# Kernel optimization log

Hardware: AMD Instinct MI355X
Metric: run time of the kernel (lower is better)

Reference implementation:

```python
import jax, jax.numpy as jnp
import numpy as np

PASS = 8        # pass_through_size
FLOW = 16       # flow_size
TRANS = FLOW - PASS  # transform_size = 8
NBINS = 64
HID = 1024


def _conditioner(yA, w1, b1, w2, b2, w3, b3):
    # MLP producing unnormalized positive bin widths Q: [B, TRANS, NBINS]
    h = jax.nn.relu(yA @ w1 + b1)
    h = jax.nn.relu(h @ w2 + b2)
    q = jax.nn.softplus(h @ w3 + b3) + 1e-6  # positivity for slopes
    return q.reshape(-1, TRANS, NBINS)


def setup_inputs() -> dict:
    key = jax.random.key(0)
    ks = jax.random.split(key, 4)
    B = 65536
    y = jax.random.uniform(ks[0], (B, FLOW + 1), dtype=jnp.float32)
    w1 = jax.random.normal(ks[1], (PASS, HID), dtype=jnp.float32) / np.sqrt(PASS)
    w2 = jax.random.normal(ks[2], (HID, HID), dtype=jnp.float32) / np.sqrt(HID)
    w3 = jax.random.normal(ks[3], (HID, TRANS * NBINS), dtype=jnp.float32) / np.sqrt(HID)
    return {
        "y": y,
        "w1": w1, "b1": jnp.zeros((HID,), jnp.float32),
        "w2": w2, "b2": jnp.zeros((HID,), jnp.float32),
        "w3": w3, "b3": jnp.zeros((TRANS * NBINS,), jnp.float32),
    }


def reference(y, w1, b1, w2, b2, w3, b3):
    yA = y[:, :PASS]                      # [B, PASS]
    yB = y[:, PASS:FLOW]                  # [B, TRANS]
    jac = y[:, FLOW:FLOW + 1]             # [B, 1]

    Q = _conditioner(yA, w1, b1, w2, b2, w3, b3)  # [B, TRANS, NBINS]
    Qsum = jnp.cumsum(Q, axis=-1)
    Qnorms = Qsum[:, :, -1:]
    Q = Q / (Qnorms / NBINS)              # slopes per bin
    Qsum = Qsum / Qnorms                  # normalized CDF knots (last == 1)

    # searchsorted(side='left') per row: count of knots strictly below value
    ybins = jnp.sum(Qsum < yB[..., None], axis=-1)          # [B, TRANS] int32
    ybins = jnp.clip(ybins, 0, NBINS - 1)                   # guard fp edge case

    paddedQsum = jnp.pad(Qsum, ((0, 0), (0, 0), (1, 0)))    # prepend 0 knot
    offsets = jnp.take_along_axis(paddedQsum, ybins[..., None], axis=-1)[..., 0]
    slopes = jnp.take_along_axis(Q, ybins[..., None], axis=-1)[..., 0]

    xB = (yB - offsets) / slopes + ybins.astype(jnp.float32) / NBINS
    jac = jac * jnp.prod(1.0 / slopes, axis=-1, keepdims=True)
    return jnp.concatenate((yA, xB, jac), axis=-1)          # [B, FLOW+1]
```

## Files before the change

### kernel.cpp

```cpp
#include <hip/hip_runtime.h>
#include <hip/hip_fp16.h>

#define HID 1024
#define QCOLS 512
#define KP 2048
#define NT 48

typedef _Float16 f16x8 __attribute__((ext_vector_type(8)));
typedef float f32x4 __attribute__((ext_vector_type(4)));

__global__ void tconv_both(const float* __restrict__ w2, __half* __restrict__ w2t,
                           const float* __restrict__ w3, __half* __restrict__ w3t) {
  __shared__ float tile[32][33];
  const int z = blockIdx.z;
  const int N = z ? QCOLS : HID;
  if (blockIdx.x * 32 >= N) return;
  const float* src = z ? w3 : w2;
  __half* dst = z ? w3t : w2t;
  int n0 = blockIdx.x * 32, k0 = blockIdx.y * 32;
  int tx = threadIdx.x, ty = threadIdx.y;
  for (int i = ty; i < 32; i += 8)
    tile[i][tx] = src[(size_t)(k0 + i) * N + n0 + tx];
  __syncthreads();
  for (int i = ty; i < 32; i += 8) {
    float v = tile[tx][i] * 256.f;
    __half h = __float2half(v);
    size_t o = (size_t)(n0 + i) * KP + k0 + tx;
    dst[o] = h;
    dst[o + 1024] = __float2half(v - __half2float(h));
  }
}

__global__ __launch_bounds__(256)
void h1k(const float* __restrict__ y, const float* __restrict__ w1,
         const float* __restrict__ b1, __half* __restrict__ h1,
         int row0, int nrows) {
  const int t = threadIdx.x & 127;
  const int rl = threadIdx.x >> 7;
  const long r = (long)blockIdx.x * 2 + rl;
  if (r >= nrows) return;
  const float* yr = y + (size_t)(row0 + r) * 17;
  float yv[8];
#pragma unroll
  for (int k = 0; k < 8; ++k) yv[k] = yr[k];
  const int c0 = t * 8;
  f32x4 a0 = *(const f32x4*)(b1 + c0);
  f32x4 a1 = *(const f32x4*)(b1 + c0 + 4);
#pragma unroll
  for (int k = 0; k < 8; ++k) {
    const f32x4 w0 = *(const f32x4*)(w1 + k * HID + c0);
    const f32x4 w1v = *(const f32x4*)(w1 + k * HID + c0 + 4);
#pragma unroll
    for (int j = 0; j < 4; ++j) {
      a0[j] = fmaf(yv[k], w0[j], a0[j]);
      a1[j] = fmaf(yv[k], w1v[j], a1[j]);
    }
  }
  f16x8 hi, lo;
#pragma unroll
  for (int j = 0; j < 8; ++j) {
    float v = fmaxf(j < 4 ? a0[j] : a1[j - 4], 0.f) * 64.f;
    _Float16 h = (_Float16)v;
    hi[j] = h;
    lo[j] = (_Float16)(v - (float)h);
  }
  *(f16x8*)(h1 + (size_t)r * KP + c0) = hi;
  *(f16x8*)(h1 + (size_t)r * KP + c0 + 1024) = lo;
}

template <int ACT>
__device__ __forceinline__
void gemm_ring_body(const __half* __restrict__ A, const __half* __restrict__ Bt,
                    const float* __restrict__ bias, __half* __restrict__ Co,
                    float* __restrict__ Cf, int ldc) {
  constexpr int SLOT = 16384 + 8192;
  __shared__ char lds[3 * SLOT];
  const int tid = threadIdx.x;
  const int lane = tid & 63, wave = tid >> 6;
  const int p = lane & 15, ql = lane >> 4;
  const int wm = wave >> 2, wn = wave & 3;

  const int gx = gridDim.x, nwg = gx * gridDim.y;
  const int bid = blockIdx.y * gx + blockIdx.x;
  const int q8 = nwg >> 3, r8 = nwg & 7;
  const int xcd = bid & 7, lxi = bid >> 3;
  const int swz = (xcd < r8 ? xcd * (q8 + 1) : r8 * (q8 + 1) + (xcd - r8) * q8) + lxi;
  const size_t row_blk = (size_t)(swz / gx) * 256;
  const size_t col_blk = (size_t)(swz % gx) * 128;

  int a_off[8], b_off[2];
#pragma unroll
  for (int m = 0; m < 8; ++m) {
    int r = wm * 128 + m * 16 + p;
    a_off[m] = r * 64 + ((ql ^ ((r >> 1) & 3)) << 4);
  }
#pragma unroll
  for (int n = 0; n < 2; ++n) {
    int r = wn * 32 + n * 16 + p;
    b_off[n] = r * 64 + ((ql ^ ((r >> 1) & 3)) << 4);
  }

  const int idx0 = tid, idx1 = tid + 512;
  const int sr0 = idx0 >> 2, sq0 = (idx0 & 3) ^ ((sr0 >> 1) & 3);
  const int sr1 = idx1 >> 2, sq1 = (idx1 & 3) ^ ((sr1 >> 1) & 3);

  auto gload = [&](const __half* g, char* l) {
    __builtin_amdgcn_global_load_lds((__attribute__((address_space(1))) void*)g,
        (__attribute__((address_space(3))) void*)l, 16, 0, 0);
  };

  auto stage = [&](int q, int slot) {
    int kt = q >> 1; if (kt > NT - 1) kt = NT - 1;
    const int h = q & 1;
    const int lk = kt * 64;
    const int ak = ((lk >= 2048) ? 1024 : 0) + (lk & 1023) + h * 32;
    const int bk = ((lk >= 1024 && lk < 2048) ? 1024 : 0) + (lk & 1023) + h * 32;
    char* base = lds + slot * SLOT;
    char* pb = base + 16384;
    gload(A + (row_blk + sr0) * (size_t)KP + ak + sq0 * 8, base + idx0 * 16);
    gload(A + (row_blk + sr1) * (size_t)KP + ak + sq1 * 8, base + idx1 * 16);
    gload(Bt + (col_blk + sr0) * (size_t)KP + bk + sq0 * 8, pb + idx0 * 16);
  };

  stage(0, 0);
  stage(1, 1);
  asm volatile("s_waitcnt vmcnt(3)" ::: "memory");
  __builtin_amdgcn_s_barrier();

  f32x4 acc[8][2] = {};

  int cur = 0;
  for (int ph = 0; ph < NT * 2; ++ph) {
    const char* base = lds + cur * SLOT;
    const char* pB = base + 16384;
    f16x8 af[8], bfr[2];
#pragma unroll
    for (int m = 0; m < 8; ++m) af[m] = *(const f16x8*)(base + a_off[m]);
#pragma unroll
    for (int n = 0; n < 2; ++n) bfr[n] = *(const f16x8*)(pB + b_off[n]);
    const int nslot = cur == 0 ? 2 : cur - 1;
    stage(ph + 2, nslot);
    __builtin_amdgcn_sched_barrier(0);
    __builtin_amdgcn_s_barrier();
    __builtin_amdgcn_sched_barrier(0);
    __builtin_amdgcn_s_setprio(1);
#pragma unroll
    for (int m = 0; m < 8; ++m)
#pragma unroll
      for (int n = 0; n < 2; ++n)
        acc[m][n] = __builtin_amdgcn_mfma_f32_16x16x32_f16(af[m], bfr[n], acc[m][n], 0, 0, 0);
    __builtin_amdgcn_s_setprio(0);
    asm volatile("s_waitcnt vmcnt(3)" ::: "memory");
    __builtin_amdgcn_sched_barrier(0);
    __builtin_amdgcn_s_barrier();
    __builtin_amdgcn_sched_barrier(0);
    cur = cur == 2 ? 0 : cur + 1;
  }

  const float unscale = 1.f / 16384.f;
#pragma unroll
  for (int n = 0; n < 2; ++n) {
    const size_t col = col_blk + wn * 32 + n * 16 + p;
    const float bv = bias[col];
#pragma unroll
    for (int m = 0; m < 8; ++m) {
      const size_t row0 = row_blk + wm * 128 + m * 16 + ql * 4;
#pragma unroll
      for (int j = 0; j < 4; ++j) {
        float v = acc[m][n][j] * unscale + bv;
        const size_t o = (row0 + j) * (size_t)ldc + col;
        if constexpr (ACT == 0) {
          float r = fmaxf(v, 0.f) * 64.f;
          __half hh = __float2half(r);
          Co[o] = hh;
          Co[o + 1024] = __float2half(r - __half2float(hh));
        } else {
          float sp = fmaxf(v, 0.f) + log1pf(expf(-fabsf(v)));
          Cf[o] = sp + 1e-6f;
        }
      }
    }
  }
}

__global__ __launch_bounds__(512, 4)
void g2relu(const __half* __restrict__ A, const __half* __restrict__ B,
            const float* __restrict__ bias, __half* __restrict__ Co) {
  gemm_ring_body<0>(A, B, bias, Co, nullptr, KP);
}

__global__ __launch_bounds__(512, 4)
void g3soft(const __half* __restrict__ A, const __half* __restrict__ B,
            const float* __restrict__ bias, float* __restrict__ Cf) {
  gemm_ring_body<1>(A, B, bias, nullptr, Cf, QCOLS);
}

__global__ __launch_bounds__(256)
void pwl_epi(const float* __restrict__ y, const float* __restrict__ q,
             float* __restrict__ out, int row0, int nrows) {
  const int wave = threadIdx.x >> 6, lane = threadIdx.x & 63;
  const int r = blockIdx.x * 4 + wave;
  if (r >= nrows) return;
  const float* yr = y + (size_t)(row0 + r) * 17;
  float* orow = out + (size_t)(row0 + r) * 17;
  const float* qr = q + (size_t)r * QCOLS;
  float prod_inv = 1.f;
#pragma unroll
  for (int t = 0; t < 8; ++t) {
    const float qv = qr[t * 64 + lane];
    float s = qv;
#pragma unroll
    for (int d = 1; d < 64; d <<= 1) {
      float u = __shfl_up(s, d);
      if (lane >= d) s += u;
    }
    const float total = __shfl(s, 63);
    const float sn = s / total;
    const float dnorm = total * 0.015625f;
    const float slope_l = qv / dnorm;
    const float yb = yr[8 + t];
    const unsigned long long m = __ballot(sn < yb);
    int bin = (int)__popcll(m);
    bin = bin > 63 ? 63 : bin;
    const float off_g = __shfl(sn, bin > 0 ? bin - 1 : 0);
    const float off = (bin == 0) ? 0.f : off_g;
    const float sl = __shfl(slope_l, bin);
    const float xB = (yb - off) / sl + (float)bin * 0.015625f;
    if (lane == t) orow[8 + t] = xB;
    prod_inv *= (1.f / sl);
  }
  if (lane < 8) orow[lane] = yr[lane];
  if (lane == 8) orow[16] = yr[16] * prod_inv;
}

extern "C" void kernel_launch(void* const* d_in, const int* in_sizes, int n_in,
                              void* d_out, int out_size, void* d_ws, size_t ws_size,
                              hipStream_t stream) {
  const float* y  = (const float*)d_in[0];
  const float* w1 = (const float*)d_in[1];
  const float* b1 = (const float*)d_in[2];
  const float* w2 = (const float*)d_in[3];
  const float* b2 = (const float*)d_in[4];
  const float* w3 = (const float*)d_in[5];
  const float* b3 = (const float*)d_in[6];
  float* out = (float*)d_out;
  const long Btot = in_sizes[0] / 17;

  char* ws = (char*)d_ws;
  __half* w2t = (__half*)ws;
  __half* w3t = (__half*)(ws + (4u << 20));
  const size_t fixed = (size_t)6 << 20;

  const size_t avail = ws_size > fixed ? ws_size - fixed : 0;
  long maxrows = (long)(avail / 8192);
  long chunk = 256;
  for (long c = 65536; c >= 256; c >>= 1) {
    if (c <= maxrows && c <= Btot) { chunk = c; break; }
  }

  __half* h1buf = (__half*)(ws + fixed);
  __half* h2buf = (__half*)(ws + fixed + (size_t)chunk * 4096);
  float* qbuf = (float*)h1buf;

  tconv_both<<<dim3(32, 32, 2), dim3(32, 8), 0, stream>>>(w2, w2t, w3, w3t);

  for (long row0 = 0; row0 < Btot; row0 += chunk) {
    const int nr = (int)((Btot - row0 < chunk) ? (Btot - row0) : chunk);
    h1k<<<(nr + 1) / 2, 256, 0, stream>>>(y, w1, b1, h1buf, (int)row0, nr);
    g2relu<<<dim3(HID / 128, nr / 256), 512, 0, stream>>>(h1buf, w2t, b2, h2buf);
    g3soft<<<dim3(QCOLS / 128, nr / 256), 512, 0, stream>>>(h2buf, w3t, b3, qbuf);
    pwl_epi<<<(nr + 3) / 4, 256, 0, stream>>>(y, qbuf, out, (int)row0, nr);
  }
}
```

Measured before the change: 917.5 us.

## Template GEMM tile shapes and move to a single-barrier ring pipeline

Parameterizes the fp16 MFMA GEMM body by block tile (BM, BN). The hidden GEMM now uses 256x256 tiles and the output GEMM 128x256 tiles, which raises operand reuse per LDS load and doubles the per-wave accumulator count. The two barriers per k-phase are merged into one wait+barrier at the top of each iteration, cutting synchronization. In exchange the larger tiles raise register pressure (launch bounds drop to 2 blocks per CU for g2) and produce fewer workgroups, which may hurt occupancy and latency hiding.

```diff
diff --git a/kernel.cpp b/kernel.cpp
--- a/kernel.cpp
+++ b/kernel.cpp
@@ -68,12 +68,17 @@
   *(f16x8*)(h1 + (size_t)r * KP + c0 + 1024) = lo;
 }
 
-template <int ACT>
+template <int ACT, int BM, int BN>
 __device__ __forceinline__
-void gemm_ring_body(const __half* __restrict__ A, const __half* __restrict__ Bt,
-                    const float* __restrict__ bias, __half* __restrict__ Co,
-                    float* __restrict__ Cf, int ldc) {
-  constexpr int SLOT = 16384 + 8192;
+void gemm1b_body(const __half* __restrict__ A, const __half* __restrict__ Bt,
+                 const float* __restrict__ bias, __half* __restrict__ Co,
+                 float* __restrict__ Cf, int ldc) {
+  constexpr int MFRAG = BM / 32;
+  constexpr int NFRAG = BN / 64;
+  constexpr int SLOT = (BM + BN) * 64;
+  constexpr int LA = BM / 128;
+  constexpr int LB = BN / 128;
+  constexpr int LPS = LA + LB;
   __shared__ char lds[3 * SLOT];
   const int tid = threadIdx.x;
   const int lane = tid & 63, wave = tid >> 6;
@@ -85,24 +90,20 @@
   const int q8 = nwg >> 3, r8 = nwg & 7;
   const int xcd = bid & 7, lxi = bid >> 3;
   const int swz = (xcd < r8 ? xcd * (q8 + 1) : r8 * (q8 + 1) + (xcd - r8) * q8) + lxi;
-  const size_t row_blk = (size_t)(swz / gx) * 256;
-  const size_t col_blk = (size_t)(swz % gx) * 128;
-
-  int a_off[8], b_off[2];
-#pragma unroll
-  for (int m = 0; m < 8; ++m) {
-    int r = wm * 128 + m * 16 + p;
+  const size_t row_blk = (size_t)(swz / gx) * BM;
+  const size_t col_blk = (size_t)(swz % gx) * BN;
+
+  int a_off[MFRAG], b_off[NFRAG];
+#pragma unroll
+  for (int m = 0; m < MFRAG; ++m) {
+    int r = wm * (BM / 2) + m * 16 + p;
     a_off[m] = r * 64 + ((ql ^ ((r >> 1) & 3)) << 4);
   }
 #pragma unroll
-  for (int n = 0; n < 2; ++n) {
-    int r = wn * 32 + n * 16 + p;
+  for (int n = 0; n < NFRAG; ++n) {
+    int r = wn * (BN / 4) + n * 16 + p;
     b_off[n] = r * 64 + ((ql ^ ((r >> 1) & 3)) << 4);
   }
-
-  const int idx0 = tid, idx1 = tid + 512;
-  const int sr0 = idx0 >> 2, sq0 = (idx0 & 3) ^ ((sr0 >> 1) & 3);
-  const int sr1 = idx1 >> 2, sq1 = (idx1 & 3) ^ ((sr1 >> 1) & 3);
 
   auto gload = [&](const __half* g, char* l) {
     __builtin_amdgcn_global_load_lds((__attribute__((address_space(1))) void*)g,
@@ -115,56 +116,65 @@
     const int lk = kt * 64;
     const int ak = ((lk >= 2048) ? 1024 : 0) + (lk & 1023) + h * 32;
     const int bk = ((lk >= 1024 && lk < 2048) ? 1024 : 0) + (lk & 1023) + h * 32;
-    char* base = lds + slot * SLOT;
-    char* pb = base + 16384;
-    gload(A + (row_blk + sr0) * (size_t)KP + ak + sq0 * 8, base + idx0 * 16);
-    gload(A + (row_blk + sr1) * (size_t)KP + ak + sq1 * 8, base + idx1 * 16);
-    gload(Bt + (col_blk + sr0) * (size_t)KP + bk + sq0 * 8, pb + idx0 * 16);
+    char* pa = lds + slot * SLOT;
+    char* pb = pa + BM * 64;
+#pragma unroll
+    for (int i = 0; i < LA; ++i) {
+      const int idx = tid + i * 512;
+      const int sr = idx >> 2, sq = (idx & 3) ^ ((sr >> 1) & 3);
+      gload(A + (row_blk + sr) * (size_t)KP + ak + sq * 8, pa + idx * 16);
+    }
+#pragma unroll
+    for (int i = 0; i < LB; ++i) {
+      const int idx = tid + i * 512;
+      const int sr = idx >> 2, sq = (idx & 3) ^ ((sr >> 1) & 3);
+      gload(Bt + (col_blk + sr) * (size_t)KP + bk + sq * 8, pb + idx * 16);
+    }
   };
 
   stage(0, 0);
   stage(1, 1);
-  asm volatile("s_waitcnt vmcnt(3)" ::: "memory");
-  __builtin_amdgcn_s_barrier();
-
-  f32x4 acc[8][2] = {};
+
+  f32x4 acc[MFRAG][NFRAG] = {};
 
   int cur = 0;
   for (int ph = 0; ph < NT * 2; ++ph) {
+    if constexpr (LPS == 4) asm volatile("s_waitcnt vmcnt(4)" ::: "memory");
+    else                    asm volatile("s_waitcnt vmcnt(3)" ::: "memory");
+    __builtin_amdgcn_sched_barrier(0);
+    __builtin_amdgcn_s_barrier();
+    __builtin_amdgcn_sched_barrier(0);
+
     const char* base = lds + cur * SLOT;
-    const char* pB = base + 16384;
-    f16x8 af[8], bfr[2];
-#pragma unroll
-    for (int m = 0; m < 8; ++m) af[m] = *(const f16x8*)(base + a_off[m]);
-#pragma unroll
-    for (int n = 0; n < 2; ++n) bfr[n] = *(const f16x8*)(pB + b_off[n]);
+    const char* pB = base + BM * 64;
+    f16x8 af[MFRAG], bfr[NFRAG];
+#pragma unroll
+    for (int m = 0; m < MFRAG; ++m) af[m] = *(const f16x8*)(base + a_off[m]);
+#pragma unroll
+    for (int n = 0; n < NFRAG; ++n) bfr[n] = *(const f16x8*)(pB + b_off[n]);
+
     const int nslot = cur == 0 ? 2 : cur - 1;
     stage(ph + 2, nslot);
     __builtin_amdgcn_sched_barrier(0);
-    __builtin_amdgcn_s_barrier();
-    __builtin_amdgcn_sched_barrier(0);
+
     __builtin_amdgcn_s_setprio(1);
 #pragma unroll
-    for (int m = 0; m < 8; ++m)
-#pragma unroll
-      for (int n = 0; n < 2; ++n)
+    for (int m = 0; m < MFRAG; ++m)
+#pragma unroll
+      for (int n = 0; n < NFRAG; ++n)
         acc[m][n] = __builtin_amdgcn_mfma_f32_16x16x32_f16(af[m], bfr[n], acc[m][n], 0, 0, 0);
     __builtin_amdgcn_s_setprio(0);
-    asm volatile("s_waitcnt vmcnt(3)" ::: "memory");
-    __builtin_amdgcn_sched_barrier(0);
-    __builtin_amdgcn_s_barrier();
-    __builtin_amdgcn_sched_barrier(0);
     cur = cur == 2 ? 0 : cur + 1;
   }
 
   const float unscale = 1.f / 16384.f;
 #pragma unroll
-  for (int n = 0; n < 2; ++n) {
-    const size_t col = col_blk + wn * 32 + n * 16 + p;
+  for (int n = 0; n < NFRAG; ++n) {
+    const size_t col = col_blk + wn * (BN / 4) + n * 16 + p;
     const float bv = bias[col];
 #pragma unroll
-    for (int m = 0; m < 8; ++m) {
-      const size_t row0 = row_blk + wm * 128 + m * 16 + ql * 4;
+    for (int m = 0; m < MFRAG; ++m) {
+      const size_t row0 = row_blk + wm * (BM / 2) + m * 16 + ql * 4;
 #pragma unroll
       for (int j = 0; j < 4; ++j) {
         float v = acc[m][n][j] * unscale + bv;
@@ -183,16 +193,16 @@
   }
 }
 
-__global__ __launch_bounds__(512, 4)
+__global__ __launch_bounds__(512, 2)
 void g2relu(const __half* __restrict__ A, const __half* __restrict__ B,
             const float* __restrict__ bias, __half* __restrict__ Co) {
-  gemm_ring_body<0>(A, B, bias, Co, nullptr, KP);
+  gemm1b_body<0, 256, 256>(A, B, bias, Co, nullptr, KP);
 }
 
 __global__ __launch_bounds__(512, 4)
 void g3soft(const __half* __restrict__ A, const __half* __restrict__ B,
             const float* __restrict__ bias, float* __restrict__ Cf) {
-  gemm_ring_body<1>(A, B, bias, nullptr, Cf, QCOLS);
+  gemm1b_body<1, 128, 256>(A, B, bias, nullptr, Cf, QCOLS);
 }
 
 __global__ __launch_bounds__(256)
@@ -267,8 +277,8 @@
   for (long row0 = 0; row0 < Btot; row0 += chunk) {
     const int nr = (int)((Btot - row0 < chunk) ? (Btot - row0) : chunk);
     h1k<<<(nr + 1) / 2, 256, 0, stream>>>(y, w1, b1, h1buf, (int)row0, nr);
-    g2relu<<<dim3(HID / 128, nr / 256), 512, 0, stream>>>(h1buf, w2t, b2, h2buf);
-    g3soft<<<dim3(QCOLS / 128, nr / 256), 512, 0, stream>>>(h2buf, w3t, b3, qbuf);
+    g2relu<<<dim3(HID / 256, nr / 256), 512, 0, stream>>>(h1buf, w2t, b2, h2buf);
+    g3soft<<<dim3(QCOLS / 256, nr / 128), 512, 0, stream>>>(h2buf, w3t, b3, qbuf);
     pwl_epi<<<(nr + 3) / 4, 256, 0, stream>>>(y, qbuf, out, (int)row0, nr);
   }
 }
```

After: 890.1 us. -3.0%, faster.
